# Kernel optimization log

Measured on AMD Instinct MI355X. Metric: run time of the kernel, lower is better.

## Reference

```python
import jax, jax.numpy as jnp
import numpy as np

D = 768          # hidden_size
M = 8            # num_patchmerges
B = 16
S = 2048         # non-CLF tokens


def setup_inputs() -> dict:
    key = jax.random.key(0)
    ks = jax.random.split(key, 12)
    std = 0.02
    tokens = jax.random.normal(ks[0], (B, 1 + S, D), dtype=jnp.float32)
    lengths = jnp.maximum(jax.random.randint(ks[1], (B,), 0, S), 1).astype(jnp.int64)
    # PatchMerger: learned queries + layernorm params
    q = jax.random.normal(ks[2], (M, D), dtype=jnp.float32) * std
    ln_scale = jnp.ones((D,), dtype=jnp.float32)
    ln_bias = jnp.zeros((D,), dtype=jnp.float32)
    # mlp1: Linear(3D, D) -> GELU -> Linear(D, D)
    w1a = jax.random.normal(ks[3], (3 * D, D), dtype=jnp.float32) * std
    b1a = jnp.zeros((D,), dtype=jnp.float32)
    w2a = jax.random.normal(ks[4], (D, D), dtype=jnp.float32) * std
    b2a = jnp.zeros((D,), dtype=jnp.float32)
    # mlp2: Linear((1+M)D, D) -> GELU -> Linear(D, D)
    w1b = jax.random.normal(ks[5], ((1 + M) * D, D), dtype=jnp.float32) * std
    b1b = jnp.zeros((D,), dtype=jnp.float32)
    w2b = jax.random.normal(ks[6], (D, D), dtype=jnp.float32) * std
    b2b = jnp.zeros((D,), dtype=jnp.float32)
    return dict(tokens=tokens, lengths=lengths, q=q, ln_scale=ln_scale,
                ln_bias=ln_bias, w1a=w1a, b1a=b1a, w2a=w2a, b2a=b2a,
                w1b=w1b, b1b=b1b, w2b=w2b, b2b=b2b)


def _hpmlp(x, w1, b1, w2, b2):
    h = jax.nn.gelu(x @ w1 + b1, approximate=False)  # dropout=0 -> identity
    return h @ w2 + b2


def _layernorm(x, scale, bias, eps=1e-5):
    mu = jnp.mean(x, axis=-1, keepdims=True)
    var = jnp.var(x, axis=-1, keepdims=True)
    return (x - mu) * jax.lax.rsqrt(var + eps) * scale + bias


def reference(tokens, lengths, q, ln_scale, ln_bias,
              w1a, b1a, w2a, b2a, w1b, b1b, w2b, b2b):
    clf = tokens[:, 0]            # [B, D]
    x = tokens[:, 1:]             # [B, S, D]
    mask = jnp.arange(S)[None, :] < lengths[:, None]   # [B, S]
    mf = mask[..., None].astype(x.dtype)

    # fixed path: masked mean / max / min over valid tokens
    denom = lengths.astype(x.dtype)[:, None]
    mean_p = jnp.sum(x * mf, axis=1) / denom
    max_p = jnp.max(jnp.where(mask[..., None], x, -jnp.inf), axis=1)
    min_p = jnp.min(jnp.where(mask[..., None], x, jnp.inf), axis=1)
    pooled_trad = jnp.concatenate([mean_p, max_p, min_p], axis=-1)  # [B, 3D]
    out_fixed = _hpmlp(pooled_trad, w1a, b1a, w2a, b2a)

    # learned path: PatchMerger (masked attention from M learned queries)
    xn = _layernorm(x, ln_scale, ln_bias)
    scores = jnp.einsum('md,bsd->bms', q, xn) / jnp.sqrt(jnp.asarray(D, x.dtype))
    scores = jnp.where(mask[:, None, :], scores, -jnp.inf)
    attn = jax.nn.softmax(scores, axis=-1)                # [B, M, S]
    merged = jnp.einsum('bms,bsd->bmd', attn, x)          # [B, M, D]
    pooled_learn = jnp.concatenate([merged.reshape(B, M * D), clf], axis=-1)
    out_learn = _hpmlp(pooled_learn, w1b, b1b, w2b, b2b)

    return jnp.concatenate([out_fixed, out_learn], axis=-1)  # [B, 2D]
```

## Files before the change

### kernel.cpp

```cpp
#include <hip/hip_runtime.h>
#include <math.h>

#define SD 768
#define SB 16
#define SM 8
#define SS 2048
#define TOK_ROW 2049
#define NEG_INF (-__builtin_inff())

#define OFF_PTRADS  0
#define OFF_PLEARN  36864
#define OFF_LTOT    147456
#define OFF_P1A     147584
#define OFF_P1B     368768
#define OFF_HA      1032320
#define OFF_HB      1044608

__device__ __forceinline__ int clen(int v) { return v < 1 ? 1 : (v > SS ? SS : v); }

__device__ __forceinline__ unsigned fenc(float f) {
  unsigned u = __float_as_uint(f);
  return (u & 0x80000000u) ? ~u : (u ^ 0x80000000u);
}
__device__ __forceinline__ float fdec(unsigned u) {
  unsigned i = (u & 0x80000000u) ? (u ^ 0x80000000u) : ~u;
  return __uint_as_float(i);
}

__global__ void k_init(float* __restrict__ ws, float* __restrict__ out,
                       const float* __restrict__ b2a, const float* __restrict__ b2b) {
  int i = blockIdx.x * 256 + threadIdx.x;
  int stride = gridDim.x * 256;
  for (int t = i; t < 147584; t += stride) {
    unsigned v = (t >= 24576 && t < 36864) ? 0xFFFFFFFFu : 0u;
    ((unsigned*)ws)[t] = v;
  }
  for (int t = i; t < 24576; t += stride) {
    int b = t / 1536, r = t - b * 1536;
    out[t] = (r < 768) ? b2a[r] : b2b[r - 768];
  }
}

__global__ __launch_bounds__(256, 2) void k1_flash(
    const float* __restrict__ tokens, const int* __restrict__ lengths,
    const float* __restrict__ q, const float* __restrict__ lns,
    const float* __restrict__ lnb, float* __restrict__ ptradS,
    float* __restrict__ plearn, float* __restrict__ ltot) {
  int c = blockIdx.x, b = blockIdx.y;
  int len = clen(lengths[b]);
  int c0 = c * 64;
  if (c0 >= len) return;
  int tid = threadIdx.x, w = tid >> 6, lane = tid & 63;
  int mm = lane & 7;

  __shared__ float p_lds[4][16][8];
  __shared__ float pool_lds[4][3][SD];
  __shared__ float O_lds[SM][SD];
  __shared__ float l_lds[4][8];

  {
    float* pf = &p_lds[0][0][0];
    for (int i = tid; i < 512; i += 256) pf[i] = 0.f;
  }

  float4 qr[8][3];
  float qs1sel, qbsel;
  {
    float4 l4[3], lb4[3];
    #pragma unroll
    for (int g = 0; g < 3; ++g) {
      l4[g] = *(const float4*)(lns + g * 256 + lane * 4);
      lb4[g] = *(const float4*)(lnb + g * 256 + lane * 4);
    }
    float qs1r[8], qbr[8];
    #pragma unroll
    for (int m = 0; m < 8; ++m) {
      float s1 = 0.f, sb = 0.f;
      #pragma unroll
      for (int g = 0; g < 3; ++g) {
        float4 qv = *(const float4*)(q + m * SD + g * 256 + lane * 4);
        float4 qs;
        qs.x = qv.x * l4[g].x; qs.y = qv.y * l4[g].y;
        qs.z = qv.z * l4[g].z; qs.w = qv.w * l4[g].w;
        qr[m][g] = qs;
        s1 += qs.x + qs.y + qs.z + qs.w;
        sb += qv.x * lb4[g].x + qv.y * lb4[g].y + qv.z * lb4[g].z + qv.w * lb4[g].w;
      }
      #pragma unroll
      for (int o = 32; o; o >>= 1) { s1 += __shfl_xor(s1, o, 64); sb += __shfl_xor(sb, o, 64); }
      qs1r[m] = s1; qbr[m] = sb;
    }
    qs1sel = qs1r[0]; qbsel = qbr[0];
    #pragma unroll
    for (int m = 1; m < 8; ++m) {
      qs1sel = (mm == m) ? qs1r[m] : qs1sel;
      qbsel = (mm == m) ? qbr[m] : qbsel;
    }
  }
  __syncthreads();

  float psum[12], pmax[12], pmin[12];
  #pragma unroll
  for (int j = 0; j < 12; ++j) { psum[j] = 0.f; pmax[j] = NEG_INF; pmin[j] = -NEG_INF; }

  int srow = c0 + w * 16;
  int smax = len - srow; if (smax > 16) smax = 16; if (smax < 0) smax = 0;
  const float* xrow = tokens + ((size_t)b * TOK_ROW + 1 + srow) * SD;
  float l_run = 0.f;

  float4 nx0 = {}, nx1 = {}, nx2 = {};
  if (smax > 0) {
    nx0 = *(const float4*)(xrow + lane * 4);
    nx1 = *(const float4*)(xrow + 256 + lane * 4);
    nx2 = *(const float4*)(xrow + 512 + lane * 4);
  }
  for (int i = 0; i < smax; ++i) {
    float4 x0 = nx0, x1 = nx1, x2 = nx2;
    if (i + 1 < smax) {
      const float* xq = xrow + (size_t)(i + 1) * SD;
      nx0 = *(const float4*)(xq + lane * 4);
      nx1 = *(const float4*)(xq + 256 + lane * 4);
      nx2 = *(const float4*)(xq + 512 + lane * 4);
    }
    float xv[12] = {x0.x, x0.y, x0.z, x0.w, x1.x, x1.y, x1.z, x1.w,
                    x2.x, x2.y, x2.z, x2.w};
    float s1 = 0.f, s2 = 0.f;
    #pragma unroll
    for (int j = 0; j < 12; ++j) {
      float v = xv[j];
      psum[j] += v;
      pmax[j] = fmaxf(pmax[j], v);
      pmin[j] = fminf(pmin[j], v);
      s1 += v;
      s2 += v * v;
    }
    float d[8];
    #pragma unroll
    for (int m = 0; m < 8; ++m) {
      float4 a0 = qr[m][0], a1 = qr[m][1], a2 = qr[m][2];
      d[m] = a0.x * xv[0] + a0.y * xv[1] + a0.z * xv[2] + a0.w * xv[3]
           + a1.x * xv[4] + a1.y * xv[5] + a1.z * xv[6] + a1.w * xv[7]
           + a2.x * xv[8] + a2.y * xv[9] + a2.z * xv[10] + a2.w * xv[11];
    }
    #pragma unroll
    for (int o = 1; o <= 4; o <<= 1)
      #pragma unroll
      for (int m = 0; m < 8; ++m) d[m] += __shfl_xor(d[m], o, 64);
    float u = d[0];
    #pragma unroll
    for (int m = 1; m < 8; ++m) u = (mm == m) ? d[m] : u;
    #pragma unroll
    for (int o = 8; o <= 32; o <<= 1) {
      u += __shfl_xor(u, o, 64);
      s1 += __shfl_xor(s1, o, 64);
      s2 += __shfl_xor(s2, o, 64);
    }
    #pragma unroll
    for (int o = 1; o <= 4; o <<= 1) { s1 += __shfl_xor(s1, o, 64); s2 += __shfl_xor(s2, o, 64); }
    float mu = s1 * (1.f / 768.f);
    float var = s2 * (1.f / 768.f) - mu * mu;
    float rstd = rsqrtf(var + 1e-5f);
    float sc = (rstd * u - rstd * mu * qs1sel + qbsel) * 0.03608439182435161f;
    float pe = __expf(sc);
    l_run += pe;
    if (lane < 8) p_lds[w][i][lane] = pe;
  }

  #pragma unroll
  for (int g = 0; g < 3; ++g) {
    int dd = g * 256 + lane * 4;
    *(float4*)&pool_lds[w][0][dd] = make_float4(psum[g*4], psum[g*4+1], psum[g*4+2], psum[g*4+3]);
    *(float4*)&pool_lds[w][1][dd] = make_float4(pmax[g*4], pmax[g*4+1], pmax[g*4+2], pmax[g*4+3]);
    *(float4*)&pool_lds[w][2][dd] = make_float4(pmin[g*4], pmin[g*4+1], pmin[g*4+2], pmin[g*4+3]);
  }
  if (lane < 8) l_lds[w][lane] = l_run;
  __syncthreads();

  if (tid < 8)
    atomicAdd(&ltot[b * 8 + tid],
              l_lds[0][tid] + l_lds[1][tid] + l_lds[2][tid] + l_lds[3][tid]);

  float O[8][12];
  #pragma unroll
  for (int m = 0; m < 8; ++m)
    #pragma unroll
    for (int j = 0; j < 12; ++j) O[m][j] = 0.f;
  float4 a0v = {}, a1v = {}, a2v = {}, b0v = {}, b1v = {}, b2v = {};
  if (smax > 0) {
    a0v = *(const float4*)(xrow + lane * 4);
    a1v = *(const float4*)(xrow + 256 + lane * 4);
    a2v = *(const float4*)(xrow + 512 + lane * 4);
  }
  if (smax > 1) {
    const float* xq = xrow + SD;
    b0v = *(const float4*)(xq + lane * 4);
    b1v = *(const float4*)(xq + 256 + lane * 4);
    b2v = *(const float4*)(xq + 512 + lane * 4);
  }
  for (int i = 0; i < smax; ++i) {
    float4 x0 = a0v, x1 = a1v, x2 = a2v;
    a0v = b0v; a1v = b1v; a2v = b2v;
    if (i + 2 < smax) {
      const float* xq = xrow + (size_t)(i + 2) * SD;
      b0v = *(const float4*)(xq + lane * 4);
      b1v = *(const float4*)(xq + 256 + lane * 4);
      b2v = *(const float4*)(xq + 512 + lane * 4);
    }
    float xv[12] = {x0.x, x0.y, x0.z, x0.w, x1.x, x1.y, x1.z, x1.w,
                    x2.x, x2.y, x2.z, x2.w};
    const float4* pr = (const float4*)&p_lds[w][i][0];
    float4 pa = pr[0], pb = pr[1];
    float pm[8] = {pa.x, pa.y, pa.z, pa.w, pb.x, pb.y, pb.z, pb.w};
    #pragma unroll
    for (int m = 0; m < 8; ++m)
      #pragma unroll
      for (int j = 0; j < 12; ++j) O[m][j] += pm[m] * xv[j];
  }
  #pragma unroll
  for (int r = 0; r < 4; ++r) {
    if (w == r) {
      #pragma unroll
      for (int m = 0; m < 8; ++m)
        #pragma unroll
        for (int g = 0; g < 3; ++g) {
          int dd = g * 256 + lane * 4;
          float4 mine = make_float4(O[m][g*4], O[m][g*4+1], O[m][g*4+2], O[m][g*4+3]);
          if (r == 0) {
            *(float4*)&O_lds[m][dd] = mine;
          } else {
            float4 cur = *(float4*)&O_lds[m][dd];
            cur.x += mine.x; cur.y += mine.y; cur.z += mine.z; cur.w += mine.w;
            *(float4*)&O_lds[m][dd] = cur;
          }
        }
    }
    __syncthreads();
  }

  {
    const float* of = &O_lds[0][0];
    for (int j = tid; j < 6144; j += 256)
      atomicAdd(&plearn[(size_t)b * 6912 + j], of[j]);
  }
  for (int j = tid; j < 768; j += 256) {
    float s = pool_lds[0][0][j] + pool_lds[1][0][j] + pool_lds[2][0][j] + pool_lds[3][0][j];
    atomicAdd(&ptradS[b * 768 + j], s);
    float mx = fmaxf(fmaxf(pool_lds[0][1][j], pool_lds[1][1][j]),
                     fmaxf(pool_lds[2][1][j], pool_lds[3][1][j]));
    atomicMax((unsigned*)&ptradS[12288 + b * 768 + j], fenc(mx));
    float mn = fminf(fminf(pool_lds[0][2][j], pool_lds[1][2][j]),
                     fminf(pool_lds[2][2][j], pool_lds[3][2][j]));
    atomicMin((unsigned*)&ptradS[24576 + b * 768 + j], fenc(mn));
  }
  if (c == 0)
    for (int dd = tid; dd < 768; dd += 256)
      plearn[(size_t)b * 6912 + 6144 + dd] = tokens[(size_t)b * TOK_ROW * SD + dd];
}

__global__ __launch_bounds__(256) void gemm_partial(
    const float* __restrict__ XA, const float* __restrict__ WA, int ktA, float* __restrict__ PA,
    const float* __restrict__ XB, const float* __restrict__ WB, float* __restrict__ PB,
    const int* __restrict__ lengths, const float* __restrict__ ltot,
    int modeA, int modeB, int epi) {
  int nt = blockIdx.x, ky = blockIdx.y;
  const float *X, *W; float* P; int kt, ktN, mode;
  if (ky < ktA) { X = XA; W = WA; P = PA; kt = ky; ktN = ktA; mode = modeA; }
  else { X = XB; W = WB; P = PB; kt = ky - ktA; ktN = gridDim.y - ktA; mode = modeB; }
  int K = ktN * 128;
  int k0 = kt * 128;
  __shared__ __align__(16) float xt[128 * 20];
  __shared__ float red[4][64][17];
  int tid = threadIdx.x;
  int kk = tid & 127, half = tid >> 7;
  #pragma unroll
  for (int u = 0; u < 8; ++u) {
    int b2 = half * 8 + u;
    float f;
    if (mode == 0) {
      int s = kt / 6;
      f = X[s * 12288 + b2 * 768 + (k0 - s * 768) + kk];
      if (s == 0) f = f / (float)clen(lengths[b2]);
      else        f = fdec(__float_as_uint(f));
    } else if (mode == 1) {
      f = X[b2 * 6912 + k0 + kk];
      if (kt < 48) f = f / ltot[b2 * 8 + (k0 / 768)];
    } else {
      f = X[b2 * K + k0 + kk];
    }
    xt[kk * 20 + b2] = f;
  }
  __syncthreads();
  int w = tid >> 6, lane = tid & 63;
  int n = nt * 64 + lane;
  float acc[16];
  #pragma unroll
  for (int b2 = 0; b2 < 16; ++b2) acc[b2] = 0.f;
  const float* Wp = W + (size_t)k0 * SD + n;
  #pragma unroll 8
  for (int kj = 0; kj < 32; ++kj) {
    int k = w + kj * 4;
    float wv = Wp[(size_t)k * SD];
    const float4* xr = reinterpret_cast<const float4*>(xt + k * 20);
    float4 a0 = xr[0], a1 = xr[1], a2 = xr[2], a3 = xr[3];
    acc[0] += wv * a0.x; acc[1] += wv * a0.y; acc[2] += wv * a0.z; acc[3] += wv * a0.w;
    acc[4] += wv * a1.x; acc[5] += wv * a1.y; acc[6] += wv * a1.z; acc[7] += wv * a1.w;
    acc[8] += wv * a2.x; acc[9] += wv * a2.y; acc[10] += wv * a2.z; acc[11] += wv * a2.w;
    acc[12] += wv * a3.x; acc[13] += wv * a3.y; acc[14] += wv * a3.z; acc[15] += wv * a3.w;
  }
  #pragma unroll
  for (int b2 = 0; b2 < 16; ++b2) red[w][lane][b2] = acc[b2];
  __syncthreads();
  for (int i = tid; i < 1024; i += 256) {
    int nn = i & 63, b2 = i >> 6;
    float r = red[0][nn][b2] + red[1][nn][b2] + red[2][nn][b2] + red[3][nn][b2];
    if (epi == 0) P[(size_t)(kt * 16 + b2) * SD + nt * 64 + nn] = r;
    else          atomicAdd(&P[b2 * 1536 + nt * 64 + nn], r);
  }
}

__global__ void gelu_reduce(const float* __restrict__ PA, const float* __restrict__ b1a,
                            float* __restrict__ HA, const float* __restrict__ PB,
                            const float* __restrict__ b1b, float* __restrict__ HB) {
  int y = blockIdx.y;
  int j = blockIdx.x * 256 + threadIdx.x;
  float r;
  if (y == 0) {
    r = b1a[j % SD];
    #pragma unroll
    for (int kt = 0; kt < 18; ++kt) r += PA[kt * 12288 + j];
    HA[j] = r * 0.5f * (1.f + erff(r * 0.70710678118654752f));
  } else {
    r = b1b[j % SD];
    #pragma unroll
    for (int kt = 0; kt < 54; ++kt) r += PB[kt * 12288 + j];
    HB[j] = r * 0.5f * (1.f + erff(r * 0.70710678118654752f));
  }
}

extern "C" void kernel_launch(void* const* d_in, const int* in_sizes, int n_in,
                              void* d_out, int out_size, void* d_ws, size_t ws_size,
                              hipStream_t stream) {
  const float* tokens = (const float*)d_in[0];
  const int* lengths  = (const int*)d_in[1];
  const float* q      = (const float*)d_in[2];
  const float* lns    = (const float*)d_in[3];
  const float* lnb    = (const float*)d_in[4];
  const float* w1a    = (const float*)d_in[5];
  const float* b1a    = (const float*)d_in[6];
  const float* w2a    = (const float*)d_in[7];
  const float* b2a    = (const float*)d_in[8];
  const float* w1b    = (const float*)d_in[9];
  const float* b1b    = (const float*)d_in[10];
  const float* w2b    = (const float*)d_in[11];
  const float* b2b    = (const float*)d_in[12];
  float* ws  = (float*)d_ws;
  float* out = (float*)d_out;

  float* ptradS = ws + OFF_PTRADS;
  float* plearn = ws + OFF_PLEARN;
  float* ltot   = ws + OFF_LTOT;
  float* p1a    = ws + OFF_P1A;
  float* p1b    = ws + OFF_P1B;
  float* ha     = ws + OFF_HA;
  float* hb     = ws + OFF_HB;

  k_init<<<dim3(128), 256, 0, stream>>>(ws, out, b2a, b2b);
  k1_flash<<<dim3(32, 16), 256, 0, stream>>>(tokens, lengths, q, lns, lnb,
                                             ptradS, plearn, ltot);
  gemm_partial<<<dim3(12, 72), 256, 0, stream>>>(ptradS, w1a, 18, p1a,
                                                 plearn, w1b, p1b,
                                                 lengths, ltot, 0, 1, 0);
  gelu_reduce<<<dim3(48, 2), 256, 0, stream>>>(p1a, b1a, ha, p1b, b1b, hb);
  gemm_partial<<<dim3(12, 12), 256, 0, stream>>>(ha, w2a, 6, out,
                                                 hb, w2b, out + 768,
                                                 lengths, ltot, 2, 2, 1);
}
```

Baseline: 219.1 us.

## Split fused pooling/attention kernel into pool and score kernels to cut registers

The single fused kernel is split in two. The first computes masked sum/max/min pooling plus per-token layernorm mean and rstd, written to a workspace buffer. The second computes attention scores and the weighted sum, keeping only 4 query vectors in registers and reading the other 4 from LDS. It also accumulates the output in two halves of 4 queries with launch bounds raised to 4 waves per SIMD, to lower register pressure and raise occupancy. The cost is an extra kernel launch, a third read of the token tensor, and per-element global atomics for pooling instead of an LDS pre-reduction.

```diff
diff --git a/kernel.cpp b/kernel.cpp
--- a/kernel.cpp
+++ b/kernel.cpp
@@ -11,10 +11,11 @@
 #define OFF_PTRADS  0
 #define OFF_PLEARN  36864
 #define OFF_LTOT    147456
-#define OFF_P1A     147584
-#define OFF_P1B     368768
-#define OFF_HA      1032320
-#define OFF_HB      1044608
+#define OFF_LNSTAT  147584
+#define OFF_P1A     213120
+#define OFF_P1B     434304
+#define OFF_HA      1097856
+#define OFF_HB      1110144
 
 __device__ __forceinline__ int clen(int v) { return v < 1 ? 1 : (v > SS ? SS : v); }
 
@@ -41,63 +42,14 @@
   }
 }
 
-__global__ __launch_bounds__(256, 2) void k1_flash(
+__global__ __launch_bounds__(256) void k_pool(
     const float* __restrict__ tokens, const int* __restrict__ lengths,
-    const float* __restrict__ q, const float* __restrict__ lns,
-    const float* __restrict__ lnb, float* __restrict__ ptradS,
-    float* __restrict__ plearn, float* __restrict__ ltot) {
+    float* __restrict__ ptradS, float* __restrict__ lnstat) {
   int c = blockIdx.x, b = blockIdx.y;
   int len = clen(lengths[b]);
   int c0 = c * 64;
   if (c0 >= len) return;
   int tid = threadIdx.x, w = tid >> 6, lane = tid & 63;
-  int mm = lane & 7;
-
-  __shared__ float p_lds[4][16][8];
-  __shared__ float pool_lds[4][3][SD];
-  __shared__ float O_lds[SM][SD];
-  __shared__ float l_lds[4][8];
-
-  {
-    float* pf = &p_lds[0][0][0];
-    for (int i = tid; i < 512; i += 256) pf[i] = 0.f;
-  }
-
-  float4 qr[8][3];
-  float qs1sel, qbsel;
-  {
-    float4 l4[3], lb4[3];
-    #pragma unroll
-    for (int g = 0; g < 3; ++g) {
-      l4[g] = *(const float4*)(lns + g * 256 + lane * 4);
-      lb4[g] = *(const float4*)(lnb + g * 256 + lane * 4);
-    }
-    float qs1r[8], qbr[8];
-    #pragma unroll
-    for (int m = 0; m < 8; ++m) {
-      float s1 = 0.f, sb = 0.f;
-      #pragma unroll
-      for (int g = 0; g < 3; ++g) {
-        float4 qv = *(const float4*)(q + m * SD + g * 256 + lane * 4);
-        float4 qs;
-        qs.x = qv.x * l4[g].x; qs.y = qv.y * l4[g].y;
-        qs.z = qv.z * l4[g].z; qs.w = qv.w * l4[g].w;
-        qr[m][g] = qs;
-        s1 += qs.x + qs.y + qs.z + qs.w;
-        sb += qv.x * lb4[g].x + qv.y * lb4[g].y + qv.z * lb4[g].z + qv.w * lb4[g].w;
-      }
-      #pragma unroll
-      for (int o = 32; o; o >>= 1) { s1 += __shfl_xor(s1, o, 64); sb += __shfl_xor(sb, o, 64); }
-      qs1r[m] = s1; qbr[m] = sb;
-    }
-    qs1sel = qs1r[0]; qbsel = qbr[0];
-    #pragma unroll
-    for (int m = 1; m < 8; ++m) {
-      qs1sel = (mm == m) ? qs1r[m] : qs1sel;
-      qbsel = (mm == m) ? qbr[m] : qbsel;
-    }
-  }
-  __syncthreads();
 
   float psum[12], pmax[12], pmin[12];
   #pragma unroll
@@ -106,7 +58,6 @@
   int srow = c0 + w * 16;
   int smax = len - srow; if (smax > 16) smax = 16; if (smax < 0) smax = 0;
   const float* xrow = tokens + ((size_t)b * TOK_ROW + 1 + srow) * SD;
-  float l_run = 0.f;
 
   float4 nx0 = {}, nx1 = {}, nx2 = {};
   if (smax > 0) {
@@ -134,123 +85,221 @@
       s1 += v;
       s2 += v * v;
     }
-    float d[8];
-    #pragma unroll
-    for (int m = 0; m < 8; ++m) {
-      float4 a0 = qr[m][0], a1 = qr[m][1], a2 = qr[m][2];
-      d[m] = a0.x * xv[0] + a0.y * xv[1] + a0.z * xv[2] + a0.w * xv[3]
-           + a1.x * xv[4] + a1.y * xv[5] + a1.z * xv[6] + a1.w * xv[7]
-           + a2.x * xv[8] + a2.y * xv[9] + a2.z * xv[10] + a2.w * xv[11];
-    }
-    #pragma unroll
-    for (int o = 1; o <= 4; o <<= 1)
-      #pragma unroll
-      for (int m = 0; m < 8; ++m) d[m] += __shfl_xor(d[m], o, 64);
-    float u = d[0];
-    #pragma unroll
-    for (int m = 1; m < 8; ++m) u = (mm == m) ? d[m] : u;
-    #pragma unroll
-    for (int o = 8; o <= 32; o <<= 1) {
-      u += __shfl_xor(u, o, 64);
-      s1 += __shfl_xor(s1, o, 64);
-      s2 += __shfl_xor(s2, o, 64);
-    }
-    #pragma unroll
-    for (int o = 1; o <= 4; o <<= 1) { s1 += __shfl_xor(s1, o, 64); s2 += __shfl_xor(s2, o, 64); }
+    #pragma unroll
+    for (int o = 1; o <= 32; o <<= 1) { s1 += __shfl_xor(s1, o, 64); s2 += __shfl_xor(s2, o, 64); }
     float mu = s1 * (1.f / 768.f);
     float var = s2 * (1.f / 768.f) - mu * mu;
     float rstd = rsqrtf(var + 1e-5f);
-    float sc = (rstd * u - rstd * mu * qs1sel + qbsel) * 0.03608439182435161f;
-    float pe = __expf(sc);
-    l_run += pe;
-    if (lane < 8) p_lds[w][i][lane] = pe;
-  }
-
-  #pragma unroll
-  for (int g = 0; g < 3; ++g) {
-    int dd = g * 256 + lane * 4;
-    *(float4*)&pool_lds[w][0][dd] = make_float4(psum[g*4], psum[g*4+1], psum[g*4+2], psum[g*4+3]);
-    *(float4*)&pool_lds[w][1][dd] = make_float4(pmax[g*4], pmax[g*4+1], pmax[g*4+2], pmax[g*4+3]);
-    *(float4*)&pool_lds[w][2][dd] = make_float4(pmin[g*4], pmin[g*4+1], pmin[g*4+2], pmin[g*4+3]);
-  }
-  if (lane < 8) l_lds[w][lane] = l_run;
+    if (lane == 0) {
+      size_t ro = ((size_t)b * SS + srow + i) * 2;
+      lnstat[ro] = mu;
+      lnstat[ro + 1] = rstd;
+    }
+  }
+
+  #pragma unroll
+  for (int j = 0; j < 12; ++j) {
+    int ch = (j >> 2) * 256 + lane * 4 + (j & 3);
+    atomicAdd(&ptradS[b * 768 + ch], psum[j]);
+    atomicMax((unsigned*)&ptradS[12288 + b * 768 + ch], fenc(pmax[j]));
+    atomicMin((unsigned*)&ptradS[24576 + b * 768 + ch], fenc(pmin[j]));
+  }
+}
+
+__global__ __launch_bounds__(256, 4) void k_score(
+    const float* __restrict__ tokens, const int* __restrict__ lengths,
+    const float* __restrict__ q, const float* __restrict__ lns,
+    const float* __restrict__ lnb, const float* __restrict__ lnstat,
+    float* __restrict__ plearn, float* __restrict__ ltot) {
+  int c = blockIdx.x, b = blockIdx.y;
+  int len = clen(lengths[b]);
+  int c0 = c * 64;
+  if (c0 >= len) return;
+  int tid = threadIdx.x, w = tid >> 6, lane = tid & 63;
+  int mm2 = lane & 3;
+
+  __shared__ float qs_lds[4][SD];
+  __shared__ float p_lds[4][16][8];
+  __shared__ float O_lds[SM][SD];
+  __shared__ float l_lds[4][8];
+
+  {
+    float* pf = &p_lds[0][0][0];
+    for (int i = tid; i < 512; i += 256) pf[i] = 0.f;
+  }
+
+  float4 qr[4][3];
+  float qs1A, qs1B, qbA, qbB;
+  {
+    float4 l4[3], lb4[3];
+    #pragma unroll
+    for (int g = 0; g < 3; ++g) {
+      l4[g] = *(const float4*)(lns + g * 256 + lane * 4);
+      lb4[g] = *(const float4*)(lnb + g * 256 + lane * 4);
+    }
+    float qs1r[8], qbr[8];
+    #pragma unroll
+    for (int m = 0; m < 8; ++m) {
+      float s1 = 0.f, sb = 0.f;
+      #pragma unroll
+      for (int g = 0; g < 3; ++g) {
+        float4 qv = *(const float4*)(q + m * SD + g * 256 + lane * 4);
+        float4 qs;
+        qs.x = qv.x * l4[g].x; qs.y = qv.y * l4[g].y;
+        qs.z = qv.z * l4[g].z; qs.w = qv.w * l4[g].w;
+        if (m < 4) qr[m][g] = qs;
+        else if (w == 0) *(float4*)&qs_lds[m - 4][g * 256 + lane * 4] = qs;
+        s1 += qs.x + qs.y + qs.z + qs.w;
+        sb += qv.x * lb4[g].x + qv.y * lb4[g].y + qv.z * lb4[g].z + qv.w * lb4[g].w;
+      }
+      #pragma unroll
+      for (int o = 32; o; o >>= 1) { s1 += __shfl_xor(s1, o, 64); sb += __shfl_xor(sb, o, 64); }
+      qs1r[m] = s1; qbr[m] = sb;
+    }
+    qs1A = qs1r[0]; qbA = qbr[0]; qs1B = qs1r[4]; qbB = qbr[4];
+    #pragma unroll
+    for (int m = 1; m < 4; ++m) {
+      qs1A = (mm2 == m) ? qs1r[m] : qs1A;
+      qbA  = (mm2 == m) ? qbr[m]  : qbA;
+      qs1B = (mm2 == m) ? qs1r[4 + m] : qs1B;
+      qbB  = (mm2 == m) ? qbr[4 + m]  : qbB;
+    }
+  }
   __syncthreads();
 
+  int srow = c0 + w * 16;
+  int smax = len - srow; if (smax > 16) smax = 16; if (smax < 0) smax = 0;
+  const float* xrow = tokens + ((size_t)b * TOK_ROW + 1 + srow) * SD;
+  const float* lrow = lnstat + ((size_t)b * SS + srow) * 2;
+  float lA = 0.f, lB = 0.f;
+
+  float4 nx0 = {}, nx1 = {}, nx2 = {};
+  float nmu = 0.f, nrs = 0.f;
+  if (smax > 0) {
+    nx0 = *(const float4*)(xrow + lane * 4);
+    nx1 = *(const float4*)(xrow + 256 + lane * 4);
+    nx2 = *(const float4*)(xrow + 512 + lane * 4);
+    nmu = lrow[0]; nrs = lrow[1];
+  }
+  for (int i = 0; i < smax; ++i) {
+    float4 x0 = nx0, x1 = nx1, x2 = nx2;
+    float mu = nmu, rstd = nrs;
+    if (i + 1 < smax) {
+      const float* xq = xrow + (size_t)(i + 1) * SD;
+      nx0 = *(const float4*)(xq + lane * 4);
+      nx1 = *(const float4*)(xq + 256 + lane * 4);
+      nx2 = *(const float4*)(xq + 512 + lane * 4);
+      nmu = lrow[2 * (i + 1)]; nrs = lrow[2 * (i + 1) + 1];
+    }
+    float xv[12] = {x0.x, x0.y, x0.z, x0.w, x1.x, x1.y, x1.z, x1.w,
+                    x2.x, x2.y, x2.z, x2.w};
+    float d[8];
+    #pragma unroll
+    for (int mq = 0; mq < 4; ++mq) {
+      float4 a0 = qr[mq][0], a1 = qr[mq][1], a2 = qr[mq][2];
+      d[mq] = a0.x * xv[0] + a0.y * xv[1] + a0.z * xv[2] + a0.w * xv[3]
+            + a1.x * xv[4] + a1.y * xv[5] + a1.z * xv[6] + a1.w * xv[7]
+            + a2.x * xv[8] + a2.y * xv[9] + a2.z * xv[10] + a2.w * xv[11];
+    }
+    #pragma unroll
+    for (int mq = 0; mq < 4; ++mq) {
+      float acc = 0.f;
+      #pragma unroll
+      for (int g = 0; g < 3; ++g) {
+        float4 qv = *(const float4*)&qs_lds[mq][g * 256 + lane * 4];
+        acc += qv.x * xv[g*4] + qv.y * xv[g*4+1] + qv.z * xv[g*4+2] + qv.w * xv[g*4+3];
+      }
+      d[4 + mq] = acc;
+    }
+    #pragma unroll
+    for (int o = 1; o <= 2; o <<= 1)
+      #pragma unroll
+      for (int m = 0; m < 8; ++m) d[m] += __shfl_xor(d[m], o, 64);
+    float uA = d[0], uB = d[4];
+    #pragma unroll
+    for (int m = 1; m < 4; ++m) {
+      uA = (mm2 == m) ? d[m] : uA;
+      uB = (mm2 == m) ? d[4 + m] : uB;
+    }
+    #pragma unroll
+    for (int o = 4; o <= 32; o <<= 1) {
+      uA += __shfl_xor(uA, o, 64);
+      uB += __shfl_xor(uB, o, 64);
+    }
+    float peA = __expf((rstd * uA - rstd * mu * qs1A + qbA) * 0.03608439182435161f);
+    float peB = __expf((rstd * uB - rstd * mu * qs1B + qbB) * 0.03608439182435161f);
+    lA += peA; lB += peB;
+    if (lane < 4) { p_lds[w][i][lane] = peA; p_lds[w][i][4 + lane] = peB; }
+  }
+  if (lane < 4) { l_lds[w][lane] = lA; l_lds[w][4 + lane] = lB; }
+  __syncthreads();
   if (tid < 8)
     atomicAdd(&ltot[b * 8 + tid],
               l_lds[0][tid] + l_lds[1][tid] + l_lds[2][tid] + l_lds[3][tid]);
 
-  float O[8][12];
-  #pragma unroll
-  for (int m = 0; m < 8; ++m)
-    #pragma unroll
-    for (int j = 0; j < 12; ++j) O[m][j] = 0.f;
-  float4 a0v = {}, a1v = {}, a2v = {}, b0v = {}, b1v = {}, b2v = {};
-  if (smax > 0) {
-    a0v = *(const float4*)(xrow + lane * 4);
-    a1v = *(const float4*)(xrow + 256 + lane * 4);
-    a2v = *(const float4*)(xrow + 512 + lane * 4);
-  }
-  if (smax > 1) {
-    const float* xq = xrow + SD;
-    b0v = *(const float4*)(xq + lane * 4);
-    b1v = *(const float4*)(xq + 256 + lane * 4);
-    b2v = *(const float4*)(xq + 512 + lane * 4);
-  }
-  for (int i = 0; i < smax; ++i) {
-    float4 x0 = a0v, x1 = a1v, x2 = a2v;
-    a0v = b0v; a1v = b1v; a2v = b2v;
-    if (i + 2 < smax) {
-      const float* xq = xrow + (size_t)(i + 2) * SD;
+  #pragma unroll
+  for (int half = 0; half < 2; ++half) {
+    float O[4][12];
+    #pragma unroll
+    for (int mq = 0; mq < 4; ++mq)
+      #pragma unroll
+      for (int j = 0; j < 12; ++j) O[mq][j] = 0.f;
+    float4 a0v = {}, a1v = {}, a2v = {}, b0v = {}, b1v = {}, b2v = {};
+    if (smax > 0) {
+      a0v = *(const float4*)(xrow + lane * 4);
+      a1v = *(const float4*)(xrow + 256 + lane * 4);
+      a2v = *(const float4*)(xrow + 512 + lane * 4);
+    }
+    if (smax > 1) {
+      const float* xq = xrow + SD;
       b0v = *(const float4*)(xq + lane * 4);
       b1v = *(const float4*)(xq + 256 + lane * 4);
       b2v = *(const float4*)(xq + 512 + lane * 4);
     }
-    float xv[12] = {x0.x, x0.y, x0.z, x0.w, x1.x, x1.y, x1.z, x1.w,
-                    x2.x, x2.y, x2.z, x2.w};
-    const float4* pr = (const float4*)&p_lds[w][i][0];
-    float4 pa = pr[0], pb = pr[1];
-    float pm[8] = {pa.x, pa.y, pa.z, pa.w, pb.x, pb.y, pb.z, pb.w};
-    #pragma unroll
-    for (int m = 0; m < 8; ++m)
-      #pragma unroll
-      for (int j = 0; j < 12; ++j) O[m][j] += pm[m] * xv[j];
-  }
-  #pragma unroll
-  for (int r = 0; r < 4; ++r) {
-    if (w == r) {
-      #pragma unroll
-      for (int m = 0; m < 8; ++m)
+    for (int i = 0; i < smax; ++i) {
+      float4 x0 = a0v, x1 = a1v, x2 = a2v;
+      a0v = b0v; a1v = b1v; a2v = b2v;
+      if (i + 2 < smax) {
+        const float* xq = xrow + (size_t)(i + 2) * SD;
+        b0v = *(const float4*)(xq + lane * 4);
+        b1v = *(const float4*)(xq + 256 + lane * 4);
+        b2v = *(const float4*)(xq + 512 + lane * 4);
+      }
+      float xv[12] = {x0.x, x0.y, x0.z, x0.w, x1.x, x1.y, x1.z, x1.w,
+                      x2.x, x2.y, x2.z, x2.w};
+      float4 pa = *(const float4*)&p_lds[w][i][half * 4];
+      float pm[4] = {pa.x, pa.y, pa.z, pa.w};
+      #pragma unroll
+      for (int mq = 0; mq < 4; ++mq)
         #pragma unroll
-        for (int g = 0; g < 3; ++g) {
-          int dd = g * 256 + lane * 4;
-          float4 mine = make_float4(O[m][g*4], O[m][g*4+1], O[m][g*4+2], O[m][g*4+3]);
-          if (r == 0) {
-            *(float4*)&O_lds[m][dd] = mine;
-          } else {
-            float4 cur = *(float4*)&O_lds[m][dd];
-            cur.x += mine.x; cur.y += mine.y; cur.z += mine.z; cur.w += mine.w;
-            *(float4*)&O_lds[m][dd] = cur;
+        for (int j = 0; j < 12; ++j) O[mq][j] += pm[mq] * xv[j];
+    }
+    #pragma unroll
+    for (int r = 0; r < 4; ++r) {
+      if (w == r) {
+        #pragma unroll
+        for (int mq = 0; mq < 4; ++mq)
+          #pragma unroll
+          for (int g = 0; g < 3; ++g) {
+            int dd = g * 256 + lane * 4;
+            float4 mine = make_float4(O[mq][g*4], O[mq][g*4+1], O[mq][g*4+2], O[mq][g*4+3]);
+            if (r == 0) {
+              *(float4*)&O_lds[half * 4 + mq][dd] = mine;
+            } else {
+              float4 cur = *(float4*)&O_lds[half * 4 + mq][dd];
+              cur.x += mine.x; cur.y += mine.y; cur.z += mine.z; cur.w += mine.w;
+              *(float4*)&O_lds[half * 4 + mq][dd] = cur;
+            }
           }
-        }
-    }
-    __syncthreads();
+      }
+      __syncthreads();
+    }
   }
 
   {
     const float* of = &O_lds[0][0];
     for (int j = tid; j < 6144; j += 256)
       atomicAdd(&plearn[(size_t)b * 6912 + j], of[j]);
-  }
-  for (int j = tid; j < 768; j += 256) {
-    float s = pool_lds[0][0][j] + pool_lds[1][0][j] + pool_lds[2][0][j] + pool_lds[3][0][j];
-    atomicAdd(&ptradS[b * 768 + j], s);
-    float mx = fmaxf(fmaxf(pool_lds[0][1][j], pool_lds[1][1][j]),
-                     fmaxf(pool_lds[2][1][j], pool_lds[3][1][j]));
-    atomicMax((unsigned*)&ptradS[12288 + b * 768 + j], fenc(mx));
-    float mn = fminf(fminf(pool_lds[0][2][j], pool_lds[1][2][j]),
-                     fminf(pool_lds[2][2][j], pool_lds[3][2][j]));
-    atomicMin((unsigned*)&ptradS[24576 + b * 768 + j], fenc(mn));
   }
   if (c == 0)
     for (int dd = tid; dd < 768; dd += 256)
@@ -359,14 +408,16 @@
   float* ptradS = ws + OFF_PTRADS;
   float* plearn = ws + OFF_PLEARN;
   float* ltot   = ws + OFF_LTOT;
+  float* lnstat = ws + OFF_LNSTAT;
   float* p1a    = ws + OFF_P1A;
   float* p1b    = ws + OFF_P1B;
   float* ha     = ws + OFF_HA;
   float* hb     = ws + OFF_HB;
 
   k_init<<<dim3(128), 256, 0, stream>>>(ws, out, b2a, b2b);
-  k1_flash<<<dim3(32, 16), 256, 0, stream>>>(tokens, lengths, q, lns, lnb,
-                                             ptradS, plearn, ltot);
+  k_pool<<<dim3(32, 16), 256, 0, stream>>>(tokens, lengths, ptradS, lnstat);
+  k_score<<<dim3(32, 16), 256, 0, stream>>>(tokens, lengths, q, lns, lnb, lnstat,
+                                            plearn, ltot);
   gemm_partial<<<dim3(12, 72), 256, 0, stream>>>(ptradS, w1a, 18, p1a,
                                                  plearn, w1b, p1b,
                                                  lengths, ltot, 0, 1, 0);
```

Result: slower. 320.1 us (+46.1%).

## Persistent work-queue kernel fusing score and accumulation in a single pass

Applied to the files above, without the earlier changes.

Replaces the two-pass per-chunk kernel with a persistent kernel of 256 blocks by 512 threads that pulls (batch, chunk) items from an atomic counter. This skips the work imbalance from variable lengths. Each wave now handles 8 rows, and scores are computed and broadcast by shuffles within one pass, so every token row is read once instead of twice. Scaled queries move from registers to LDS, which frees registers. The cost is LDS reads per row, extra per-item barriers and an 8-way reduction.

```diff
diff --git a/kernel.cpp b/kernel.cpp
--- a/kernel.cpp
+++ b/kernel.cpp
@@ -15,6 +15,9 @@
 #define OFF_P1B     368768
 #define OFF_HA      1032320
 #define OFF_HB      1044608
+#define OFF_CNT     1056896
+
+#define NITEM 512
 
 __device__ __forceinline__ int clen(int v) { return v < 1 ? 1 : (v > SS ? SS : v); }
 
@@ -39,222 +42,202 @@
     int b = t / 1536, r = t - b * 1536;
     out[t] = (r < 768) ? b2a[r] : b2b[r - 768];
   }
-}
-
-__global__ __launch_bounds__(256, 2) void k1_flash(
+  if (i == 0) ((int*)ws)[OFF_CNT] = 0;
+}
+
+__global__ __launch_bounds__(512, 1) void k_fused(
     const float* __restrict__ tokens, const int* __restrict__ lengths,
     const float* __restrict__ q, const float* __restrict__ lns,
     const float* __restrict__ lnb, float* __restrict__ ptradS,
-    float* __restrict__ plearn, float* __restrict__ ltot) {
-  int c = blockIdx.x, b = blockIdx.y;
-  int len = clen(lengths[b]);
-  int c0 = c * 64;
-  if (c0 >= len) return;
+    float* __restrict__ plearn, float* __restrict__ ltot,
+    int* __restrict__ cnt) {
+  __shared__ float q_lds[8][SD];
+  __shared__ float O_lds[SM][SD];
+  __shared__ float pool_lds[8][3][SD];
+  __shared__ float l_lds[8][8];
+  __shared__ float qmeta[16];
+  __shared__ int item_s;
   int tid = threadIdx.x, w = tid >> 6, lane = tid & 63;
-  int mm = lane & 7;
-
-  __shared__ float p_lds[4][16][8];
-  __shared__ float pool_lds[4][3][SD];
-  __shared__ float O_lds[SM][SD];
-  __shared__ float l_lds[4][8];
+  int mm2 = lane & 3;
 
   {
-    float* pf = &p_lds[0][0][0];
-    for (int i = tid; i < 512; i += 256) pf[i] = 0.f;
-  }
-
-  float4 qr[8][3];
-  float qs1sel, qbsel;
-  {
-    float4 l4[3], lb4[3];
+    float s1 = 0.f, sb = 0.f;
     #pragma unroll
     for (int g = 0; g < 3; ++g) {
-      l4[g] = *(const float4*)(lns + g * 256 + lane * 4);
-      lb4[g] = *(const float4*)(lnb + g * 256 + lane * 4);
-    }
-    float qs1r[8], qbr[8];
-    #pragma unroll
-    for (int m = 0; m < 8; ++m) {
-      float s1 = 0.f, sb = 0.f;
-      #pragma unroll
-      for (int g = 0; g < 3; ++g) {
-        float4 qv = *(const float4*)(q + m * SD + g * 256 + lane * 4);
-        float4 qs;
-        qs.x = qv.x * l4[g].x; qs.y = qv.y * l4[g].y;
-        qs.z = qv.z * l4[g].z; qs.w = qv.w * l4[g].w;
-        qr[m][g] = qs;
-        s1 += qs.x + qs.y + qs.z + qs.w;
-        sb += qv.x * lb4[g].x + qv.y * lb4[g].y + qv.z * lb4[g].z + qv.w * lb4[g].w;
-      }
-      #pragma unroll
-      for (int o = 32; o; o >>= 1) { s1 += __shfl_xor(s1, o, 64); sb += __shfl_xor(sb, o, 64); }
-      qs1r[m] = s1; qbr[m] = sb;
-    }
-    qs1sel = qs1r[0]; qbsel = qbr[0];
-    #pragma unroll
-    for (int m = 1; m < 8; ++m) {
-      qs1sel = (mm == m) ? qs1r[m] : qs1sel;
-      qbsel = (mm == m) ? qbr[m] : qbsel;
-    }
+      float4 l4  = *(const float4*)(lns + g * 256 + lane * 4);
+      float4 lb4 = *(const float4*)(lnb + g * 256 + lane * 4);
+      float4 qv  = *(const float4*)(q + w * SD + g * 256 + lane * 4);
+      float4 qs = make_float4(qv.x * l4.x, qv.y * l4.y, qv.z * l4.z, qv.w * l4.w);
+      *(float4*)&q_lds[w][g * 256 + lane * 4] = qs;
+      s1 += qs.x + qs.y + qs.z + qs.w;
+      sb += qv.x * lb4.x + qv.y * lb4.y + qv.z * lb4.z + qv.w * lb4.w;
+    }
+    #pragma unroll
+    for (int o = 32; o; o >>= 1) { s1 += __shfl_xor(s1, o, 64); sb += __shfl_xor(sb, o, 64); }
+    if (lane == 0) { qmeta[w] = s1; qmeta[8 + w] = sb; }
   }
   __syncthreads();
-
-  float psum[12], pmax[12], pmin[12];
-  #pragma unroll
-  for (int j = 0; j < 12; ++j) { psum[j] = 0.f; pmax[j] = NEG_INF; pmin[j] = -NEG_INF; }
-
-  int srow = c0 + w * 16;
-  int smax = len - srow; if (smax > 16) smax = 16; if (smax < 0) smax = 0;
-  const float* xrow = tokens + ((size_t)b * TOK_ROW + 1 + srow) * SD;
-  float l_run = 0.f;
-
-  float4 nx0 = {}, nx1 = {}, nx2 = {};
-  if (smax > 0) {
-    nx0 = *(const float4*)(xrow + lane * 4);
-    nx1 = *(const float4*)(xrow + 256 + lane * 4);
-    nx2 = *(const float4*)(xrow + 512 + lane * 4);
-  }
-  for (int i = 0; i < smax; ++i) {
-    float4 x0 = nx0, x1 = nx1, x2 = nx2;
-    if (i + 1 < smax) {
-      const float* xq = xrow + (size_t)(i + 1) * SD;
-      nx0 = *(const float4*)(xq + lane * 4);
-      nx1 = *(const float4*)(xq + 256 + lane * 4);
-      nx2 = *(const float4*)(xq + 512 + lane * 4);
-    }
-    float xv[12] = {x0.x, x0.y, x0.z, x0.w, x1.x, x1.y, x1.z, x1.w,
-                    x2.x, x2.y, x2.z, x2.w};
-    float s1 = 0.f, s2 = 0.f;
-    #pragma unroll
-    for (int j = 0; j < 12; ++j) {
-      float v = xv[j];
-      psum[j] += v;
-      pmax[j] = fmaxf(pmax[j], v);
-      pmin[j] = fminf(pmin[j], v);
-      s1 += v;
-      s2 += v * v;
-    }
-    float d[8];
-    #pragma unroll
-    for (int m = 0; m < 8; ++m) {
-      float4 a0 = qr[m][0], a1 = qr[m][1], a2 = qr[m][2];
-      d[m] = a0.x * xv[0] + a0.y * xv[1] + a0.z * xv[2] + a0.w * xv[3]
-           + a1.x * xv[4] + a1.y * xv[5] + a1.z * xv[6] + a1.w * xv[7]
-           + a2.x * xv[8] + a2.y * xv[9] + a2.z * xv[10] + a2.w * xv[11];
-    }
-    #pragma unroll
-    for (int o = 1; o <= 4; o <<= 1)
-      #pragma unroll
-      for (int m = 0; m < 8; ++m) d[m] += __shfl_xor(d[m], o, 64);
-    float u = d[0];
-    #pragma unroll
-    for (int m = 1; m < 8; ++m) u = (mm == m) ? d[m] : u;
-    #pragma unroll
-    for (int o = 8; o <= 32; o <<= 1) {
-      u += __shfl_xor(u, o, 64);
-      s1 += __shfl_xor(s1, o, 64);
-      s2 += __shfl_xor(s2, o, 64);
-    }
-    #pragma unroll
-    for (int o = 1; o <= 4; o <<= 1) { s1 += __shfl_xor(s1, o, 64); s2 += __shfl_xor(s2, o, 64); }
-    float mu = s1 * (1.f / 768.f);
-    float var = s2 * (1.f / 768.f) - mu * mu;
-    float rstd = rsqrtf(var + 1e-5f);
-    float sc = (rstd * u - rstd * mu * qs1sel + qbsel) * 0.03608439182435161f;
-    float pe = __expf(sc);
-    l_run += pe;
-    if (lane < 8) p_lds[w][i][lane] = pe;
-  }
-
-  #pragma unroll
-  for (int g = 0; g < 3; ++g) {
-    int dd = g * 256 + lane * 4;
-    *(float4*)&pool_lds[w][0][dd] = make_float4(psum[g*4], psum[g*4+1], psum[g*4+2], psum[g*4+3]);
-    *(float4*)&pool_lds[w][1][dd] = make_float4(pmax[g*4], pmax[g*4+1], pmax[g*4+2], pmax[g*4+3]);
-    *(float4*)&pool_lds[w][2][dd] = make_float4(pmin[g*4], pmin[g*4+1], pmin[g*4+2], pmin[g*4+3]);
-  }
-  if (lane < 8) l_lds[w][lane] = l_run;
-  __syncthreads();
-
-  if (tid < 8)
-    atomicAdd(&ltot[b * 8 + tid],
-              l_lds[0][tid] + l_lds[1][tid] + l_lds[2][tid] + l_lds[3][tid]);
-
-  float O[8][12];
-  #pragma unroll
-  for (int m = 0; m < 8; ++m)
-    #pragma unroll
-    for (int j = 0; j < 12; ++j) O[m][j] = 0.f;
-  float4 a0v = {}, a1v = {}, a2v = {}, b0v = {}, b1v = {}, b2v = {};
-  if (smax > 0) {
-    a0v = *(const float4*)(xrow + lane * 4);
-    a1v = *(const float4*)(xrow + 256 + lane * 4);
-    a2v = *(const float4*)(xrow + 512 + lane * 4);
-  }
-  if (smax > 1) {
-    const float* xq = xrow + SD;
-    b0v = *(const float4*)(xq + lane * 4);
-    b1v = *(const float4*)(xq + 256 + lane * 4);
-    b2v = *(const float4*)(xq + 512 + lane * 4);
-  }
-  for (int i = 0; i < smax; ++i) {
-    float4 x0 = a0v, x1 = a1v, x2 = a2v;
-    a0v = b0v; a1v = b1v; a2v = b2v;
-    if (i + 2 < smax) {
-      const float* xq = xrow + (size_t)(i + 2) * SD;
-      b0v = *(const float4*)(xq + lane * 4);
-      b1v = *(const float4*)(xq + 256 + lane * 4);
-      b2v = *(const float4*)(xq + 512 + lane * 4);
-    }
-    float xv[12] = {x0.x, x0.y, x0.z, x0.w, x1.x, x1.y, x1.z, x1.w,
-                    x2.x, x2.y, x2.z, x2.w};
-    const float4* pr = (const float4*)&p_lds[w][i][0];
-    float4 pa = pr[0], pb = pr[1];
-    float pm[8] = {pa.x, pa.y, pa.z, pa.w, pb.x, pb.y, pb.z, pb.w};
+  float qs1A = qmeta[mm2],     qs1B = qmeta[4 + mm2];
+  float qbA  = qmeta[8 + mm2], qbB  = qmeta[12 + mm2];
+  const float KS = 0.03608439182435161f;
+
+  for (;;) {
+    __syncthreads();
+    if (tid == 0) item_s = atomicAdd(cnt, 1);
+    __syncthreads();
+    int item = item_s;
+    if (item >= NITEM) break;
+    int b = item >> 5, c = item & 31;
+    int len = clen(lengths[b]);
+    int c0 = c * 64;
+    if (c0 >= len) continue;
+
+    int srow = c0 + w * 8;
+    int smax = len - srow; if (smax > 8) smax = 8; if (smax < 0) smax = 0;
+    const float* xrow = tokens + ((size_t)b * TOK_ROW + 1 + srow) * SD;
+
+    float psum[12], pmx[12], pmn[12];
+    #pragma unroll
+    for (int j = 0; j < 12; ++j) { psum[j] = 0.f; pmx[j] = NEG_INF; pmn[j] = -NEG_INF; }
+    float O[8][12];
     #pragma unroll
     for (int m = 0; m < 8; ++m)
       #pragma unroll
-      for (int j = 0; j < 12; ++j) O[m][j] += pm[m] * xv[j];
-  }
-  #pragma unroll
-  for (int r = 0; r < 4; ++r) {
-    if (w == r) {
+      for (int j = 0; j < 12; ++j) O[m][j] = 0.f;
+    float lA = 0.f, lB = 0.f;
+
+    float4 nx0 = {}, nx1 = {}, nx2 = {};
+    if (smax > 0) {
+      nx0 = *(const float4*)(xrow + lane * 4);
+      nx1 = *(const float4*)(xrow + 256 + lane * 4);
+      nx2 = *(const float4*)(xrow + 512 + lane * 4);
+    }
+    for (int i = 0; i < smax; ++i) {
+      float4 x0 = nx0, x1 = nx1, x2 = nx2;
+      if (i + 1 < smax) {
+        const float* xq = xrow + (size_t)(i + 1) * SD;
+        nx0 = *(const float4*)(xq + lane * 4);
+        nx1 = *(const float4*)(xq + 256 + lane * 4);
+        nx2 = *(const float4*)(xq + 512 + lane * 4);
+      }
+      float xv[12] = {x0.x, x0.y, x0.z, x0.w, x1.x, x1.y, x1.z, x1.w,
+                      x2.x, x2.y, x2.z, x2.w};
+      float s1 = 0.f, s2 = 0.f;
+      #pragma unroll
+      for (int j = 0; j < 12; ++j) {
+        float v = xv[j];
+        psum[j] += v;
+        pmx[j] = fmaxf(pmx[j], v);
+        pmn[j] = fminf(pmn[j], v);
+        s1 += v;
+        s2 += v * v;
+      }
+      float d[8];
+      #pragma unroll
+      for (int m = 0; m < 8; ++m) {
+        float4 q0 = *(const float4*)&q_lds[m][lane * 4];
+        float4 q1 = *(const float4*)&q_lds[m][256 + lane * 4];
+        float4 q2 = *(const float4*)&q_lds[m][512 + lane * 4];
+        d[m] = q0.x * xv[0] + q0.y * xv[1] + q0.z * xv[2] + q0.w * xv[3]
+             + q1.x * xv[4] + q1.y * xv[5] + q1.z * xv[6] + q1.w * xv[7]
+             + q2.x * xv[8] + q2.y * xv[9] + q2.z * xv[10] + q2.w * xv[11];
+      }
+      #pragma unroll
+      for (int o = 1; o <= 2; o <<= 1)
+        #pragma unroll
+        for (int m = 0; m < 8; ++m) d[m] += __shfl_xor(d[m], o, 64);
+      float uA = d[0], uB = d[4];
+      #pragma unroll
+      for (int m = 1; m < 4; ++m) {
+        uA = (mm2 == m) ? d[m] : uA;
+        uB = (mm2 == m) ? d[4 + m] : uB;
+      }
+      #pragma unroll
+      for (int o = 4; o <= 32; o <<= 1) {
+        uA += __shfl_xor(uA, o, 64);
+        uB += __shfl_xor(uB, o, 64);
+        s1 += __shfl_xor(s1, o, 64);
+        s2 += __shfl_xor(s2, o, 64);
+      }
+      #pragma unroll
+      for (int o = 1; o <= 2; o <<= 1) { s1 += __shfl_xor(s1, o, 64); s2 += __shfl_xor(s2, o, 64); }
+      float mu = s1 * (1.f / 768.f);
+      float var = s2 * (1.f / 768.f) - mu * mu;
+      float rstd = rsqrtf(var + 1e-5f);
+      float peA = __expf((rstd * uA - rstd * mu * qs1A + qbA) * KS);
+      float peB = __expf((rstd * uB - rstd * mu * qs1B + qbB) * KS);
+      lA += peA; lB += peB;
+      float pm[8];
+      #pragma unroll
+      for (int m = 0; m < 4; ++m) {
+        pm[m]     = __shfl(peA, m, 4);
+        pm[4 + m] = __shfl(peB, m, 4);
+      }
       #pragma unroll
       for (int m = 0; m < 8; ++m)
         #pragma unroll
-        for (int g = 0; g < 3; ++g) {
-          int dd = g * 256 + lane * 4;
-          float4 mine = make_float4(O[m][g*4], O[m][g*4+1], O[m][g*4+2], O[m][g*4+3]);
-          if (r == 0) {
-            *(float4*)&O_lds[m][dd] = mine;
-          } else {
-            float4 cur = *(float4*)&O_lds[m][dd];
-            cur.x += mine.x; cur.y += mine.y; cur.z += mine.z; cur.w += mine.w;
-            *(float4*)&O_lds[m][dd] = cur;
+        for (int j = 0; j < 12; ++j) O[m][j] += pm[m] * xv[j];
+    }
+
+    if (lane < 4) { l_lds[w][lane] = lA; l_lds[w][4 + lane] = lB; }
+    #pragma unroll
+    for (int g = 0; g < 3; ++g) {
+      int dd = g * 256 + lane * 4;
+      *(float4*)&pool_lds[w][0][dd] = make_float4(psum[g*4], psum[g*4+1], psum[g*4+2], psum[g*4+3]);
+      *(float4*)&pool_lds[w][1][dd] = make_float4(pmx[g*4], pmx[g*4+1], pmx[g*4+2], pmx[g*4+3]);
+      *(float4*)&pool_lds[w][2][dd] = make_float4(pmn[g*4], pmn[g*4+1], pmn[g*4+2], pmn[g*4+3]);
+    }
+    __syncthreads();
+
+    if (tid < 8) {
+      float lt = 0.f;
+      #pragma unroll
+      for (int ww = 0; ww < 8; ++ww) lt += l_lds[ww][tid];
+      atomicAdd(&ltot[b * 8 + tid], lt);
+    }
+
+    #pragma unroll
+    for (int r = 0; r < 8; ++r) {
+      if (w == r) {
+        #pragma unroll
+        for (int m = 0; m < 8; ++m)
+          #pragma unroll
+          for (int g = 0; g < 3; ++g) {
+            int dd = g * 256 + lane * 4;
+            float4 mine = make_float4(O[m][g*4], O[m][g*4+1], O[m][g*4+2], O[m][g*4+3]);
+            if (r == 0) {
+              *(float4*)&O_lds[m][dd] = mine;
+            } else {
+              float4 cur = *(float4*)&O_lds[m][dd];
+              cur.x += mine.x; cur.y += mine.y; cur.z += mine.z; cur.w += mine.w;
+              *(float4*)&O_lds[m][dd] = cur;
+            }
           }
-        }
-    }
-    __syncthreads();
-  }
-
-  {
-    const float* of = &O_lds[0][0];
-    for (int j = tid; j < 6144; j += 256)
-      atomicAdd(&plearn[(size_t)b * 6912 + j], of[j]);
-  }
-  for (int j = tid; j < 768; j += 256) {
-    float s = pool_lds[0][0][j] + pool_lds[1][0][j] + pool_lds[2][0][j] + pool_lds[3][0][j];
-    atomicAdd(&ptradS[b * 768 + j], s);
-    float mx = fmaxf(fmaxf(pool_lds[0][1][j], pool_lds[1][1][j]),
-                     fmaxf(pool_lds[2][1][j], pool_lds[3][1][j]));
-    atomicMax((unsigned*)&ptradS[12288 + b * 768 + j], fenc(mx));
-    float mn = fminf(fminf(pool_lds[0][2][j], pool_lds[1][2][j]),
-                     fminf(pool_lds[2][2][j], pool_lds[3][2][j]));
-    atomicMin((unsigned*)&ptradS[24576 + b * 768 + j], fenc(mn));
-  }
-  if (c == 0)
-    for (int dd = tid; dd < 768; dd += 256)
-      plearn[(size_t)b * 6912 + 6144 + dd] = tokens[(size_t)b * TOK_ROW * SD + dd];
+      }
+      __syncthreads();
+    }
+
+    {
+      const float* of = &O_lds[0][0];
+      for (int j = tid; j < 6144; j += 512)
+        atomicAdd(&plearn[(size_t)b * 6912 + j], of[j]);
+    }
+    for (int j = tid; j < 768; j += 512) {
+      float s = 0.f, mx = NEG_INF, mn = -NEG_INF;
+      #pragma unroll
+      for (int ww = 0; ww < 8; ++ww) {
+        s += pool_lds[ww][0][j];
+        mx = fmaxf(mx, pool_lds[ww][1][j]);
+        mn = fminf(mn, pool_lds[ww][2][j]);
+      }
+      atomicAdd(&ptradS[b * 768 + j], s);
+      atomicMax((unsigned*)&ptradS[12288 + b * 768 + j], fenc(mx));
+      atomicMin((unsigned*)&ptradS[24576 + b * 768 + j], fenc(mn));
+    }
+    if (c == 0)
+      for (int dd = tid; dd < 768; dd += 512)
+        plearn[(size_t)b * 6912 + 6144 + dd] = tokens[(size_t)b * TOK_ROW * SD + dd];
+  }
 }
 
 __global__ __launch_bounds__(256) void gemm_partial(
@@ -363,10 +346,11 @@
   float* p1b    = ws + OFF_P1B;
   float* ha     = ws + OFF_HA;
   float* hb     = ws + OFF_HB;
+  int*   cnt    = (int*)(ws + OFF_CNT);
 
   k_init<<<dim3(128), 256, 0, stream>>>(ws, out, b2a, b2b);
-  k1_flash<<<dim3(32, 16), 256, 0, stream>>>(tokens, lengths, q, lns, lnb,
-                                             ptradS, plearn, ltot);
+  k_fused<<<dim3(256), 512, 0, stream>>>(tokens, lengths, q, lns, lnb,
+                                         ptradS, plearn, ltot, cnt);
   gemm_partial<<<dim3(12, 72), 256, 0, stream>>>(ptradS, w1a, 18, p1a,
                                                  plearn, w1b, p1b,
                                                  lengths, ltot, 0, 1, 0);
```

New measurement: 239.1 us. 1.09x slower.
